# Kernel tuning notes

Measured on AMD Instinct MI355X. Metric: run time of the kernel, lower is better.

## Reference

```python
import jax, jax.numpy as jnp
import numpy as np

BN_EPS = 1e-3  # keras BatchNormalization default epsilon


def setup_inputs() -> dict:
    key = jax.random.key(0)
    ks = jax.random.split(key, 8)
    B, F, Df = 256, 64, 256   # batch, num_features, feature_dim
    E, H, D = 8, 256, 256     # num_experts, hidden, expert_dim
    s1 = 1.0 / np.sqrt(Df)
    s2 = 1.0 / np.sqrt(H)
    return {
        "x":  jax.random.normal(ks[0], (B, F, Df), jnp.float32),
        "Wr": jax.random.normal(ks[1], (Df, E), jnp.float32) * s1,
        "br": jnp.zeros((E,), jnp.float32),
        "W1": jax.random.normal(ks[2], (E, Df, H), jnp.float32) * s1,
        "b1": jnp.zeros((E, H), jnp.float32),
        "g1": jnp.ones((E, H), jnp.float32),
        "be1": jnp.zeros((E, H), jnp.float32),
        "m1": jnp.zeros((E, H), jnp.float32),
        "v1": jnp.ones((E, H), jnp.float32),
        "W2": jax.random.normal(ks[3], (E, H, H), jnp.float32) * s2,
        "b2": jnp.zeros((E, H), jnp.float32),
        "g2": jnp.ones((E, H), jnp.float32),
        "be2": jnp.zeros((E, H), jnp.float32),
        "m2": jnp.zeros((E, H), jnp.float32),
        "v2": jnp.ones((E, H), jnp.float32),
        "Wo": jax.random.normal(ks[4], (E, H, D), jnp.float32) * s2,
        "bo": jnp.zeros((E, D), jnp.float32),
    }


def _bn(h, g, b, m, v):
    # inference-mode batch norm with moving stats; params are [E,H], h is [B,F,E,H]
    return g * (h - m) * jax.lax.rsqrt(v + BN_EPS) + b


def reference(x, Wr, br, W1, b1, g1, be1, m1, v1,
              W2, b2, g2, be2, m2, v2, Wo, bo):
    # learned softmax routing: mean over batch -> [F, Df] -> dense -> softmax
    feat = jnp.mean(x, axis=0)                     # [F, Df]
    w = jax.nn.softmax(feat @ Wr + br, axis=-1)    # [F, E]

    # all experts at once: Dense -> BN -> relu, x2, then Dense output
    h = jnp.einsum('bfd,edh->bfeh', x, W1) + b1    # [B, F, E, H]
    h = jax.nn.relu(_bn(h, g1, be1, m1, v1))
    h = jnp.einsum('bfeh,ehk->bfek', h, W2) + b2
    h = jax.nn.relu(_bn(h, g2, be2, m2, v2))
    y = jnp.einsum('bfeh,ehd->bfed', h, Wo) + bo   # [B, F, E, D]

    # weighted combine over experts (routing weights broadcast over batch)
    return jnp.einsum('bfed,fe->bfd', y, w)        # [B, F, D]
```

## Files before the change

kernel.cpp:

```cpp
#include <hip/hip_runtime.h>
#include <hip/hip_bf16.h>
#include <stdint.h>

#define BN_EPS 1e-3f

typedef __bf16 bf16x8 __attribute__((ext_vector_type(8)));
typedef float  f32x16 __attribute__((ext_vector_type(16)));

static constexpr size_t WS_FOLD_OFF = 24ull * 131072ull;
static constexpr size_t WS_WRT_OFF  = WS_FOLD_OFF + 32768ull;
static constexpr size_t WS_WB_OFF   = WS_WRT_OFF + 2048ull;

__global__ __launch_bounds__(256) void fold_kernel(
    const float* __restrict__ b1, const float* __restrict__ g1, const float* __restrict__ be1,
    const float* __restrict__ m1, const float* __restrict__ v1,
    const float* __restrict__ b2, const float* __restrict__ g2, const float* __restrict__ be2,
    const float* __restrict__ m2, const float* __restrict__ v2,
    float* __restrict__ fold) {
  int i = blockIdx.x * 256 + threadIdx.x;
  if (i < 2048) {
    float s1 = g1[i] * rsqrtf(v1[i] + BN_EPS);
    fold[i]        = s1;
    fold[2048 + i] = (b1[i] - m1[i]) * s1 + be1[i];
    float s2 = g2[i] * rsqrtf(v2[i] + BN_EPS);
    fold[4096 + i] = s2;
    fold[6144 + i] = (b2[i] - m2[i]) * s2 + be2[i];
  }
}

__global__ __launch_bounds__(256) void pack_kernel(
    const float* __restrict__ W1, const float* __restrict__ W2, const float* __restrict__ Wo,
    __bf16* __restrict__ pk) {
  __shared__ float sl[16 * 256];
  int bid = blockIdx.x;
  int m = bid >> 4, ks = bid & 15;
  int L = m >> 3, e = m & 7;
  const float* Ws = (L == 0 ? W1 : (L == 1 ? W2 : Wo)) + (size_t)e * 65536 + (size_t)ks * 16 * 256;
  int t = threadIdx.x;
#pragma unroll
  for (int it = 0; it < 4; ++it) {
    int el4 = it * 256 + t;
    float4 v = *reinterpret_cast<const float4*>(Ws + (size_t)el4 * 4);
    *reinterpret_cast<float4*>(&sl[el4 * 4]) = v;
  }
  __syncthreads();
#pragma unroll
  for (int it = 0; it < 2; ++it) {
    int task = it * 256 + t;
    int nb = task >> 6, l = task & 63;
    int colb = nb * 32 + (l & 31);
    int krow = (l >> 5) * 8;
    union { __bf16 h[8]; int4 v; } u;
#pragma unroll
    for (int i = 0; i < 8; ++i) u.h[i] = (__bf16)sl[(krow + i) * 256 + colb];
    size_t off = ((size_t)(m * 8 + nb) * 16 + ks) * 512 + (size_t)l * 8;
    *reinterpret_cast<int4*>(pk + off) = u.v;
  }
}

__global__ __launch_bounds__(256) void route_kernel(
    const float* __restrict__ x, const float* __restrict__ Wr, const float* __restrict__ br,
    const float* __restrict__ bo, float* __restrict__ wrt, float* __restrict__ wb) {
  __shared__ float feat[256];
  __shared__ float lg[8];
  __shared__ float wsm[8];
  int f = blockIdx.x, t = threadIdx.x;
  float acc = 0.f;
  const float* xp = x + (size_t)f * 256 + t;
  for (int b = 0; b < 256; ++b) acc += xp[(size_t)b * 16384];
  feat[t] = acc * (1.0f / 256.0f);
  __syncthreads();
  if (t < 8) {
    float a = br[t];
    for (int d = 0; d < 256; ++d) a += feat[d] * Wr[d * 8 + t];
    lg[t] = a;
  }
  __syncthreads();
  if (t == 0) {
    float mx = lg[0];
#pragma unroll
    for (int e = 1; e < 8; ++e) mx = fmaxf(mx, lg[e]);
    float ex[8]; float s = 0.f;
#pragma unroll
    for (int e = 0; e < 8; ++e) { ex[e] = expf(lg[e] - mx); s += ex[e]; }
    float inv = 1.0f / s;
#pragma unroll
    for (int e = 0; e < 8; ++e) { float v = ex[e] * inv; wsm[e] = v; wrt[f * 8 + e] = v; }
  }
  __syncthreads();
  float o = 0.f;
#pragma unroll
  for (int e = 0; e < 8; ++e) o += wsm[e] * bo[e * 256 + t];
  wb[f * 256 + t] = o;
}

__global__ __launch_bounds__(512, 2) void moe_kernel(
    const float* __restrict__ x, const __bf16* __restrict__ pk,
    const float* __restrict__ fold, const float* __restrict__ wrt,
    const float* __restrict__ wb, float* __restrict__ out) {
  __shared__ char xb[32768];
  __shared__ char h1[32768];
  __shared__ char h2[32768];
  const int tid = threadIdx.x;
  const int l = tid & 63, w = tid >> 6;
  const int l31 = l & 31, hi = l >> 5;
  const int b = blockIdx.x;

  {
    const float* xg = x + (size_t)b * 16384;
#pragma unroll
    for (int it = 0; it < 8; ++it) {
      int el4 = it * 512 + tid;
      int token = el4 >> 6;
      int k4 = (el4 & 63) * 4;
      float4 v = *reinterpret_cast<const float4*>(xg + (size_t)el4 * 4);
      union { __bf16 h[4]; short4 s; } u;
      u.h[0] = (__bf16)v.x; u.h[1] = (__bf16)v.y; u.h[2] = (__bf16)v.z; u.h[3] = (__bf16)v.w;
      int addr = (((k4 >> 3) * 64 + token) << 4) + ((k4 & 4) << 1);
      *reinterpret_cast<short4*>(xb + addr) = u.s;
    }
  }

  f32x16 outacc[2];
#pragma unroll
  for (int mt = 0; mt < 2; ++mt)
#pragma unroll
    for (int r = 0; r < 16; ++r) outacc[mt][r] = 0.f;

  __syncthreads();

#define FRAG(buf, fr, tok) (*reinterpret_cast<const bf16x8*>((buf) + ((((fr) * 64) + (tok)) << 4)))

#pragma unroll 1
  for (int e = 0; e < 8; ++e) {
    {
      f32x16 a0, a1;
#pragma unroll
      for (int r = 0; r < 16; ++r) { a0[r] = 0.f; a1[r] = 0.f; }
      const __bf16* pb = pk + (size_t)((0 * 8 + e) * 8 + w) * 8192;
#pragma unroll
      for (int ks = 0; ks < 16; ++ks) {
        bf16x8 wf = *reinterpret_cast<const bf16x8*>(pb + (size_t)ks * 512 + (size_t)l * 8);
        bf16x8 x0 = FRAG(xb, 2 * ks + hi, l31);
        bf16x8 x1 = FRAG(xb, 2 * ks + hi, 32 + l31);
        a0 = __builtin_amdgcn_mfma_f32_32x32x16_bf16(wf, x0, a0, 0, 0, 0);
        a1 = __builtin_amdgcn_mfma_f32_32x32x16_bf16(wf, x1, a1, 0, 0, 0);
      }
      const float* sA = fold + 0 * 4096 + e * 256 + w * 32 + 4 * hi;
      const float* cA = sA + 2048;
#pragma unroll
      for (int g = 0; g < 4; ++g) {
        float4 s4 = *reinterpret_cast<const float4*>(sA + 8 * g);
        float4 c4 = *reinterpret_cast<const float4*>(cA + 8 * g);
        union { __bf16 h[4]; uint2 u; } p0, p1;
#pragma unroll
        for (int j = 0; j < 4; ++j) {
          float sj = (&s4.x)[j], cj = (&c4.x)[j];
          p0.h[j] = (__bf16)fmaxf(a0[4 * g + j] * sj + cj, 0.f);
          p1.h[j] = (__bf16)fmaxf(a1[4 * g + j] * sj + cj, 0.f);
        }
        int addr = (((w * 4 + g) * 64 + l31) << 4) + hi * 8;
        *reinterpret_cast<uint2*>(h1 + addr) = p0.u;
        *reinterpret_cast<uint2*>(h1 + addr + 512) = p1.u;
      }
    }
    __syncthreads();

    {
      f32x16 a0, a1;
#pragma unroll
      for (int r = 0; r < 16; ++r) { a0[r] = 0.f; a1[r] = 0.f; }
      const __bf16* pb = pk + (size_t)((1 * 8 + e) * 8 + w) * 8192;
#pragma unroll
      for (int ks = 0; ks < 16; ++ks) {
        bf16x8 wf = *reinterpret_cast<const bf16x8*>(pb + (size_t)ks * 512 + (size_t)l * 8);
        bf16x8 x0 = FRAG(h1, 2 * ks + hi, l31);
        bf16x8 x1 = FRAG(h1, 2 * ks + hi, 32 + l31);
        a0 = __builtin_amdgcn_mfma_f32_32x32x16_bf16(wf, x0, a0, 0, 0, 0);
        a1 = __builtin_amdgcn_mfma_f32_32x32x16_bf16(wf, x1, a1, 0, 0, 0);
      }
      const float* sA = fold + 1 * 4096 + e * 256 + w * 32 + 4 * hi;
      const float* cA = sA + 2048;
#pragma unroll
      for (int g = 0; g < 4; ++g) {
        float4 s4 = *reinterpret_cast<const float4*>(sA + 8 * g);
        float4 c4 = *reinterpret_cast<const float4*>(cA + 8 * g);
        union { __bf16 h[4]; uint2 u; } p0, p1;
#pragma unroll
        for (int j = 0; j < 4; ++j) {
          float sj = (&s4.x)[j], cj = (&c4.x)[j];
          p0.h[j] = (__bf16)fmaxf(a0[4 * g + j] * sj + cj, 0.f);
          p1.h[j] = (__bf16)fmaxf(a1[4 * g + j] * sj + cj, 0.f);
        }
        int addr = (((w * 4 + g) * 64 + l31) << 4) + hi * 8;
        *reinterpret_cast<uint2*>(h2 + addr) = p0.u;
        *reinterpret_cast<uint2*>(h2 + addr + 512) = p1.u;
      }
    }
    __syncthreads();

    {
      f32x16 a0, a1;
#pragma unroll
      for (int r = 0; r < 16; ++r) { a0[r] = 0.f; a1[r] = 0.f; }
      const __bf16* pb = pk + (size_t)((2 * 8 + e) * 8 + w) * 8192;
#pragma unroll
      for (int ks = 0; ks < 16; ++ks) {
        bf16x8 bfr = *reinterpret_cast<const bf16x8*>(pb + (size_t)ks * 512 + (size_t)l * 8);
        bf16x8 h0 = FRAG(h2, 2 * ks + hi, l31);
        bf16x8 hm = FRAG(h2, 2 * ks + hi, 32 + l31);
        a0 = __builtin_amdgcn_mfma_f32_32x32x16_bf16(h0, bfr, a0, 0, 0, 0);
        a1 = __builtin_amdgcn_mfma_f32_32x32x16_bf16(hm, bfr, a1, 0, 0, 0);
      }
#pragma unroll
      for (int mt = 0; mt < 2; ++mt) {
        const f32x16& am = (mt == 0) ? a0 : a1;
#pragma unroll
        for (int r = 0; r < 16; ++r) {
          int row = mt * 32 + 4 * hi + (r & 3) + 8 * (r >> 2);
          float wv = wrt[row * 8 + e];
          outacc[mt][r] += wv * am[r];
        }
      }
    }
  }

  float* og = out + (size_t)b * 16384;
  const int col = w * 32 + l31;
#pragma unroll
  for (int mt = 0; mt < 2; ++mt) {
#pragma unroll
    for (int r = 0; r < 16; ++r) {
      int row = mt * 32 + 4 * hi + (r & 3) + 8 * (r >> 2);
      og[row * 256 + col] = outacc[mt][r] + wb[row * 256 + col];
    }
  }
#undef FRAG
}

extern "C" void kernel_launch(void* const* d_in, const int* in_sizes, int n_in,
                              void* d_out, int out_size, void* d_ws, size_t ws_size,
                              hipStream_t stream) {
  const float* x   = (const float*)d_in[0];
  const float* Wr  = (const float*)d_in[1];
  const float* br  = (const float*)d_in[2];
  const float* W1  = (const float*)d_in[3];
  const float* b1  = (const float*)d_in[4];
  const float* g1  = (const float*)d_in[5];
  const float* be1 = (const float*)d_in[6];
  const float* m1  = (const float*)d_in[7];
  const float* v1  = (const float*)d_in[8];
  const float* W2  = (const float*)d_in[9];
  const float* b2  = (const float*)d_in[10];
  const float* g2  = (const float*)d_in[11];
  const float* be2 = (const float*)d_in[12];
  const float* m2  = (const float*)d_in[13];
  const float* v2  = (const float*)d_in[14];
  const float* Wo  = (const float*)d_in[15];
  const float* bo  = (const float*)d_in[16];
  float* out = (float*)d_out;

  __bf16* pk  = (__bf16*)d_ws;
  float* fold = (float*)((char*)d_ws + WS_FOLD_OFF);
  float* wrt  = (float*)((char*)d_ws + WS_WRT_OFF);
  float* wb   = (float*)((char*)d_ws + WS_WB_OFF);

  hipLaunchKernelGGL(fold_kernel, dim3(8), dim3(256), 0, stream,
                     b1, g1, be1, m1, v1, b2, g2, be2, m2, v2, fold);
  hipLaunchKernelGGL(pack_kernel, dim3(384), dim3(256), 0, stream, W1, W2, Wo, pk);
  hipLaunchKernelGGL(route_kernel, dim3(64), dim3(256), 0, stream, x, Wr, br, bo, wrt, wb);
  hipLaunchKernelGGL(moe_kernel, dim3(256), dim3(512), 0, stream, x, pk, fold, wrt, wb, out);
}
```

Before: 105.9 us.

## Tile 128 tokens per block, split experts across two blocks with atomic combine

The MoE kernel now processes 128 tokens (two batch rows) per block, so each weight fragment loaded from global memory feeds four MFMAs instead of two. Experts are split in half across block pairs and the partial sums are combined with atomic adds into a zeroed output. Weight fragments are prefetched one k-step ahead, and the hidden activations reuse a single LDS buffer with an extra barrier. The routing reduction is vectorised across four batch partitions. The change adds a memset, atomic traffic and larger LDS use, which may lower occupancy.

```diff
diff --git a/kernel.cpp b/kernel.cpp
--- a/kernel.cpp
+++ b/kernel.cpp
@@ -61,14 +61,28 @@
 __global__ __launch_bounds__(256) void route_kernel(
     const float* __restrict__ x, const float* __restrict__ Wr, const float* __restrict__ br,
     const float* __restrict__ bo, float* __restrict__ wrt, float* __restrict__ wb) {
+  __shared__ float4 part[4][64];
   __shared__ float feat[256];
   __shared__ float lg[8];
   __shared__ float wsm[8];
   int f = blockIdx.x, t = threadIdx.x;
-  float acc = 0.f;
-  const float* xp = x + (size_t)f * 256 + t;
-  for (int b = 0; b < 256; ++b) acc += xp[(size_t)b * 16384];
-  feat[t] = acc * (1.0f / 256.0f);
+  int bq = t >> 6, dq = t & 63;
+  float4 s = {0.f, 0.f, 0.f, 0.f};
+  const float* xp = x + (size_t)(bq * 64) * 16384 + f * 256 + dq * 4;
+  for (int bi = 0; bi < 64; ++bi) {
+    float4 v = *reinterpret_cast<const float4*>(xp + (size_t)bi * 16384);
+    s.x += v.x; s.y += v.y; s.z += v.z; s.w += v.w;
+  }
+  part[bq][dq] = s;
+  __syncthreads();
+  if (t < 64) {
+    float4 a = part[0][t], b = part[1][t], c = part[2][t], d = part[3][t];
+    float4 r;
+    r.x = (a.x + b.x) + (c.x + d.x); r.y = (a.y + b.y) + (c.y + d.y);
+    r.z = (a.z + b.z) + (c.z + d.z); r.w = (a.w + b.w) + (c.w + d.w);
+    r.x *= (1.f/256.f); r.y *= (1.f/256.f); r.z *= (1.f/256.f); r.w *= (1.f/256.f);
+    *reinterpret_cast<float4*>(&feat[t * 4]) = r;
+  }
   __syncthreads();
   if (t < 8) {
     float a = br[t];
@@ -80,10 +94,10 @@
     float mx = lg[0];
 #pragma unroll
     for (int e = 1; e < 8; ++e) mx = fmaxf(mx, lg[e]);
-    float ex[8]; float s = 0.f;
-#pragma unroll
-    for (int e = 0; e < 8; ++e) { ex[e] = expf(lg[e] - mx); s += ex[e]; }
-    float inv = 1.0f / s;
+    float ex[8]; float sum = 0.f;
+#pragma unroll
+    for (int e = 0; e < 8; ++e) { ex[e] = expf(lg[e] - mx); sum += ex[e]; }
+    float inv = 1.0f / sum;
 #pragma unroll
     for (int e = 0; e < 8; ++e) { float v = ex[e] * inv; wsm[e] = v; wrt[f * 8 + e] = v; }
   }
@@ -92,150 +106,137 @@
 #pragma unroll
   for (int e = 0; e < 8; ++e) o += wsm[e] * bo[e * 256 + t];
   wb[f * 256 + t] = o;
+}
+
+__device__ __forceinline__ void phase_swapped(
+    const char* __restrict__ src, char* __restrict__ dst,
+    const __bf16* __restrict__ pb, const float* __restrict__ sA, const float* __restrict__ cA,
+    int l, int l31, int hi, int w) {
+  f32x16 acc[4];
+#pragma unroll
+  for (int mt = 0; mt < 4; ++mt)
+#pragma unroll
+    for (int r = 0; r < 16; ++r) acc[mt][r] = 0.f;
+  bf16x8 bq = *reinterpret_cast<const bf16x8*>(pb + (size_t)l * 8);
+#pragma unroll
+  for (int ks = 0; ks < 16; ++ks) {
+    bf16x8 bn = (ks < 15) ? *reinterpret_cast<const bf16x8*>(pb + (size_t)(ks + 1) * 512 + (size_t)l * 8) : bq;
+#pragma unroll
+    for (int mt = 0; mt < 4; ++mt) {
+      bf16x8 xf = *reinterpret_cast<const bf16x8*>(src + (((2 * ks + hi) * 128 + mt * 32 + l31) << 4));
+      acc[mt] = __builtin_amdgcn_mfma_f32_32x32x16_bf16(bq, xf, acc[mt], 0, 0, 0);
+    }
+    bq = bn;
+  }
+  __syncthreads();
+#pragma unroll
+  for (int g = 0; g < 4; ++g) {
+    float4 s4 = *reinterpret_cast<const float4*>(sA + 8 * g);
+    float4 c4 = *reinterpret_cast<const float4*>(cA + 8 * g);
+#pragma unroll
+    for (int mt = 0; mt < 4; ++mt) {
+      union { __bf16 h[4]; uint2 u; } p;
+#pragma unroll
+      for (int j = 0; j < 4; ++j) {
+        float sj = (&s4.x)[j], cj = (&c4.x)[j];
+        p.h[j] = (__bf16)fmaxf(acc[mt][4 * g + j] * sj + cj, 0.f);
+      }
+      int addr = (((w * 4 + g) * 128 + mt * 32 + l31) << 4) + hi * 8;
+      *reinterpret_cast<uint2*>(dst + addr) = p.u;
+    }
+  }
+  __syncthreads();
 }
 
 __global__ __launch_bounds__(512, 2) void moe_kernel(
     const float* __restrict__ x, const __bf16* __restrict__ pk,
     const float* __restrict__ fold, const float* __restrict__ wrt,
     const float* __restrict__ wb, float* __restrict__ out) {
-  __shared__ char xb[32768];
-  __shared__ char h1[32768];
-  __shared__ char h2[32768];
+  __shared__ char xb[65536];
+  __shared__ char hb[65536];
+  __shared__ float wrts[512];
   const int tid = threadIdx.x;
   const int l = tid & 63, w = tid >> 6;
   const int l31 = l & 31, hi = l >> 5;
-  const int b = blockIdx.x;
+  const int bid = blockIdx.x;
+  const int tile = bid >> 1, eh = bid & 1;
 
   {
-    const float* xg = x + (size_t)b * 16384;
-#pragma unroll
-    for (int it = 0; it < 8; ++it) {
-      int el4 = it * 512 + tid;
-      int token = el4 >> 6;
-      int k4 = (el4 & 63) * 4;
-      float4 v = *reinterpret_cast<const float4*>(xg + (size_t)el4 * 4);
-      union { __bf16 h[4]; short4 s; } u;
-      u.h[0] = (__bf16)v.x; u.h[1] = (__bf16)v.y; u.h[2] = (__bf16)v.z; u.h[3] = (__bf16)v.w;
-      int addr = (((k4 >> 3) * 64 + token) << 4) + ((k4 & 4) << 1);
-      *reinterpret_cast<short4*>(xb + addr) = u.s;
-    }
-  }
-
-  f32x16 outacc[2];
-#pragma unroll
-  for (int mt = 0; mt < 2; ++mt)
+    const float* xg = x + (size_t)tile * 32768;
+    int tok = w * 16 + (l & 15);
+    int kc = l >> 4;
+#pragma unroll
+    for (int i = 0; i < 8; ++i) {
+      int fr = kc * 8 + i;
+      const float* src = xg + (size_t)tok * 256 + fr * 8;
+      float4 v0 = *reinterpret_cast<const float4*>(src);
+      float4 v1 = *reinterpret_cast<const float4*>(src + 4);
+      union { __bf16 h[8]; int4 v; } u;
+      u.h[0] = (__bf16)v0.x; u.h[1] = (__bf16)v0.y; u.h[2] = (__bf16)v0.z; u.h[3] = (__bf16)v0.w;
+      u.h[4] = (__bf16)v1.x; u.h[5] = (__bf16)v1.y; u.h[6] = (__bf16)v1.z; u.h[7] = (__bf16)v1.w;
+      *reinterpret_cast<int4*>(xb + ((fr * 128 + tok) << 4)) = u.v;
+    }
+  }
+  if (tid < 512) wrts[tid] = wrt[tid];
+
+  f32x16 outacc[4];
+#pragma unroll
+  for (int mt = 0; mt < 4; ++mt)
 #pragma unroll
     for (int r = 0; r < 16; ++r) outacc[mt][r] = 0.f;
 
   __syncthreads();
 
-#define FRAG(buf, fr, tok) (*reinterpret_cast<const bf16x8*>((buf) + ((((fr) * 64) + (tok)) << 4)))
-
 #pragma unroll 1
-  for (int e = 0; e < 8; ++e) {
+  for (int ep = 0; ep < 4; ++ep) {
+    const int e = eh * 4 + ep;
+    phase_swapped(xb, hb, pk + (size_t)((0 * 8 + e) * 8 + w) * 8192,
+                  fold + 0 * 4096 + e * 256 + w * 32 + 4 * hi,
+                  fold + 0 * 4096 + 2048 + e * 256 + w * 32 + 4 * hi, l, l31, hi, w);
+    phase_swapped(hb, hb, pk + (size_t)((1 * 8 + e) * 8 + w) * 8192,
+                  fold + 1 * 4096 + e * 256 + w * 32 + 4 * hi,
+                  fold + 1 * 4096 + 2048 + e * 256 + w * 32 + 4 * hi, l, l31, hi, w);
     {
-      f32x16 a0, a1;
-#pragma unroll
-      for (int r = 0; r < 16; ++r) { a0[r] = 0.f; a1[r] = 0.f; }
-      const __bf16* pb = pk + (size_t)((0 * 8 + e) * 8 + w) * 8192;
+      f32x16 acc[4];
+#pragma unroll
+      for (int mt = 0; mt < 4; ++mt)
+#pragma unroll
+        for (int r = 0; r < 16; ++r) acc[mt][r] = 0.f;
+      const __bf16* pb = pk + (size_t)((2 * 8 + e) * 8 + w) * 8192;
+      bf16x8 bq = *reinterpret_cast<const bf16x8*>(pb + (size_t)l * 8);
 #pragma unroll
       for (int ks = 0; ks < 16; ++ks) {
-        bf16x8 wf = *reinterpret_cast<const bf16x8*>(pb + (size_t)ks * 512 + (size_t)l * 8);
-        bf16x8 x0 = FRAG(xb, 2 * ks + hi, l31);
-        bf16x8 x1 = FRAG(xb, 2 * ks + hi, 32 + l31);
-        a0 = __builtin_amdgcn_mfma_f32_32x32x16_bf16(wf, x0, a0, 0, 0, 0);
-        a1 = __builtin_amdgcn_mfma_f32_32x32x16_bf16(wf, x1, a1, 0, 0, 0);
+        bf16x8 bn = (ks < 15) ? *reinterpret_cast<const bf16x8*>(pb + (size_t)(ks + 1) * 512 + (size_t)l * 8) : bq;
+#pragma unroll
+        for (int mt = 0; mt < 4; ++mt) {
+          bf16x8 hf = *reinterpret_cast<const bf16x8*>(hb + (((2 * ks + hi) * 128 + mt * 32 + l31) << 4));
+          acc[mt] = __builtin_amdgcn_mfma_f32_32x32x16_bf16(hf, bq, acc[mt], 0, 0, 0);
+        }
+        bq = bn;
       }
-      const float* sA = fold + 0 * 4096 + e * 256 + w * 32 + 4 * hi;
-      const float* cA = sA + 2048;
-#pragma unroll
-      for (int g = 0; g < 4; ++g) {
-        float4 s4 = *reinterpret_cast<const float4*>(sA + 8 * g);
-        float4 c4 = *reinterpret_cast<const float4*>(cA + 8 * g);
-        union { __bf16 h[4]; uint2 u; } p0, p1;
-#pragma unroll
-        for (int j = 0; j < 4; ++j) {
-          float sj = (&s4.x)[j], cj = (&c4.x)[j];
-          p0.h[j] = (__bf16)fmaxf(a0[4 * g + j] * sj + cj, 0.f);
-          p1.h[j] = (__bf16)fmaxf(a1[4 * g + j] * sj + cj, 0.f);
-        }
-        int addr = (((w * 4 + g) * 64 + l31) << 4) + hi * 8;
-        *reinterpret_cast<uint2*>(h1 + addr) = p0.u;
-        *reinterpret_cast<uint2*>(h1 + addr + 512) = p1.u;
-      }
-    }
-    __syncthreads();
-
-    {
-      f32x16 a0, a1;
-#pragma unroll
-      for (int r = 0; r < 16; ++r) { a0[r] = 0.f; a1[r] = 0.f; }
-      const __bf16* pb = pk + (size_t)((1 * 8 + e) * 8 + w) * 8192;
-#pragma unroll
-      for (int ks = 0; ks < 16; ++ks) {
-        bf16x8 wf = *reinterpret_cast<const bf16x8*>(pb + (size_t)ks * 512 + (size_t)l * 8);
-        bf16x8 x0 = FRAG(h1, 2 * ks + hi, l31);
-        bf16x8 x1 = FRAG(h1, 2 * ks + hi, 32 + l31);
-        a0 = __builtin_amdgcn_mfma_f32_32x32x16_bf16(wf, x0, a0, 0, 0, 0);
-        a1 = __builtin_amdgcn_mfma_f32_32x32x16_bf16(wf, x1, a1, 0, 0, 0);
-      }
-      const float* sA = fold + 1 * 4096 + e * 256 + w * 32 + 4 * hi;
-      const float* cA = sA + 2048;
-#pragma unroll
-      for (int g = 0; g < 4; ++g) {
-        float4 s4 = *reinterpret_cast<const float4*>(sA + 8 * g);
-        float4 c4 = *reinterpret_cast<const float4*>(cA + 8 * g);
-        union { __bf16 h[4]; uint2 u; } p0, p1;
-#pragma unroll
-        for (int j = 0; j < 4; ++j) {
-          float sj = (&s4.x)[j], cj = (&c4.x)[j];
-          p0.h[j] = (__bf16)fmaxf(a0[4 * g + j] * sj + cj, 0.f);
-          p1.h[j] = (__bf16)fmaxf(a1[4 * g + j] * sj + cj, 0.f);
-        }
-        int addr = (((w * 4 + g) * 64 + l31) << 4) + hi * 8;
-        *reinterpret_cast<uint2*>(h2 + addr) = p0.u;
-        *reinterpret_cast<uint2*>(h2 + addr + 512) = p1.u;
-      }
-    }
-    __syncthreads();
-
-    {
-      f32x16 a0, a1;
-#pragma unroll
-      for (int r = 0; r < 16; ++r) { a0[r] = 0.f; a1[r] = 0.f; }
-      const __bf16* pb = pk + (size_t)((2 * 8 + e) * 8 + w) * 8192;
-#pragma unroll
-      for (int ks = 0; ks < 16; ++ks) {
-        bf16x8 bfr = *reinterpret_cast<const bf16x8*>(pb + (size_t)ks * 512 + (size_t)l * 8);
-        bf16x8 h0 = FRAG(h2, 2 * ks + hi, l31);
-        bf16x8 hm = FRAG(h2, 2 * ks + hi, 32 + l31);
-        a0 = __builtin_amdgcn_mfma_f32_32x32x16_bf16(h0, bfr, a0, 0, 0, 0);
-        a1 = __builtin_amdgcn_mfma_f32_32x32x16_bf16(hm, bfr, a1, 0, 0, 0);
-      }
-#pragma unroll
-      for (int mt = 0; mt < 2; ++mt) {
-        const f32x16& am = (mt == 0) ? a0 : a1;
+#pragma unroll
+      for (int mt = 0; mt < 4; ++mt) {
 #pragma unroll
         for (int r = 0; r < 16; ++r) {
           int row = mt * 32 + 4 * hi + (r & 3) + 8 * (r >> 2);
-          float wv = wrt[row * 8 + e];
-          outacc[mt][r] += wv * am[r];
+          outacc[mt][r] += wrts[(row & 63) * 8 + e] * acc[mt][r];
         }
       }
     }
   }
 
-  float* og = out + (size_t)b * 16384;
+  float* og = out + (size_t)tile * 32768;
   const int col = w * 32 + l31;
 #pragma unroll
-  for (int mt = 0; mt < 2; ++mt) {
+  for (int mt = 0; mt < 4; ++mt) {
 #pragma unroll
     for (int r = 0; r < 16; ++r) {
       int row = mt * 32 + 4 * hi + (r & 3) + 8 * (r >> 2);
-      og[row * 256 + col] = outacc[mt][r] + wb[row * 256 + col];
-    }
-  }
-#undef FRAG
+      float v = outacc[mt][r];
+      if (eh == 0) v += wb[(row & 63) * 256 + col];
+      unsafeAtomicAdd(og + row * 256 + col, v);
+    }
+  }
 }
 
 extern "C" void kernel_launch(void* const* d_in, const int* in_sizes, int n_in,
@@ -265,6 +266,7 @@
   float* wrt  = (float*)((char*)d_ws + WS_WRT_OFF);
   float* wb   = (float*)((char*)d_ws + WS_WB_OFF);
 
+  hipMemsetAsync(out, 0, (size_t)out_size * sizeof(float), stream);
   hipLaunchKernelGGL(fold_kernel, dim3(8), dim3(256), 0, stream,
                      b1, g1, be1, m1, v1, b2, g2, be2, m2, v2, fold);
   hipLaunchKernelGGL(pack_kernel, dim3(384), dim3(256), 0, stream, W1, W2, Wo, pk);
```

Result: slower. 115.9 us (+9.5%).
